# Kernel tuning notes

Measured on AMD Instinct MI355X. Metric: run time of the kernel, lower is better.

The kernel has to match this reference:

```python
import jax, jax.numpy as jnp
import numpy as np

USER_NUM = 200000
ITEM_NUM = 100000
N_NODES = USER_NUM + ITEM_NUM
EMB = 64
NNZ = 12800000
N_LAYERS = 3


def setup_inputs() -> dict:
    key = jax.random.key(0)
    k1, k2, k3, k4, k5 = jax.random.split(key, 5)
    user_emb = jax.random.normal(k1, (USER_NUM, EMB), dtype=jnp.float32) * 0.1
    item_emb = jax.random.normal(k2, (ITEM_NUM, EMB), dtype=jnp.float32) * 0.1
    adj_rows = jax.random.randint(k3, (NNZ,), 0, N_NODES, dtype=jnp.int32)
    adj_cols = jax.random.randint(k4, (NNZ,), 0, N_NODES, dtype=jnp.int32)
    # values of a symmetrically-normalized Laplacian are ~1/sqrt(d_i d_j);
    # avg degree ~= NNZ / N_NODES ~= 43, so scale uniform values accordingly
    # to keep row sums near 1 (numerically faithful to a normalized adjacency)
    adj_vals = jax.random.uniform(k5, (NNZ,), dtype=jnp.float32) * (2.0 * N_NODES / NNZ)
    return {
        "user_emb": user_emb,
        "item_emb": item_emb,
        "adj_vals": adj_vals,
        "adj_rows": adj_rows,
        "adj_cols": adj_cols,
    }


def reference(user_emb, item_emb, adj_vals, adj_rows, adj_cols):
    n_users = user_emb.shape[0]
    n_items = item_emb.shape[0]
    n_nodes = n_users + n_items

    # ego_embeddings = cat([user_emb, item_emb], 0)
    ego = jnp.concatenate([user_emb, item_emb], axis=0)  # [N, d]

    # Running accumulation replaces stack+mean over layer outputs.
    acc = ego
    for _ in range(N_LAYERS):
        # SpMM: out[r] += v * ego[c] for each nonzero (r, c, v)
        gathered = ego[adj_cols] * adj_vals[:, None]          # [nnz, d]
        ego = jax.ops.segment_sum(gathered, adj_rows, num_segments=n_nodes)
        acc = acc + ego

    all_emb = acc / jnp.asarray(N_LAYERS + 1, dtype=acc.dtype)  # mean over layers
    user_all = all_emb[:n_users]
    item_all = all_emb[n_users:]
    return (user_all, item_all)
```

## Files before the change

### kernel.cpp

```cpp
#include <hip/hip_runtime.h>


typedef unsigned short u16;
typedef unsigned int   u32;
typedef unsigned long long u64;

#define USER_ELEMS   (200000 * 64)
#define N_NODES      300000
#define EMB          64
#define NNZ          12800000
#define TOTAL_ELEMS  (N_NODES * EMB)

#define NBUCK    2048
#define ROWS_PB  147
#define EPB      65536
#define NB_A     196
#define CNT_LEN  (NBUCK * NB_A)
#define TILE     4096
#define NTILES   (EPB / TILE)
#define BCAP     6784

#define FLAGS_SZ   256ULL
#define ACC_SZ     76800000ULL
#define EGO_SZ     38400000ULL
#define RP_SZ      1200128ULL
#define BS_SZ      1024ULL
#define CNTM_SZ    1605632ULL
#define COL_SZ     51200000ULL
#define VALSORT_SZ 25600000ULL
#define BIG_SZ     115200000ULL
#define PERM_SZ    51200000ULL
#define LAYER_SZ   76800000ULL

#define T0_NEED (FLAGS_SZ + CNTM_SZ + 2*BS_SZ + COL_SZ + VALSORT_SZ + RP_SZ + BIG_SZ)
#define T2_NEED (FLAGS_SZ + ACC_SZ + EGO_SZ + 2*RP_SZ + 2*BS_SZ + PERM_SZ)

__device__ __forceinline__ float bf2f(u16 b) {
    return __uint_as_float(((u32)b) << 16);
}
__device__ __forceinline__ u16 f2bf(float f) {
    u32 u = __float_as_uint(f);
    u32 r = (u + 0x7fffu + ((u >> 16) & 1u)) >> 16;
    return (u16)r;
}

__global__ void k_detect(const u16* __restrict__ emb, const u16* __restrict__ vals,
                         int* __restrict__ flags) {
    int lane = threadIdx.x;
    u16 a = emb[lane * 2];
    int ea = (a >> 7) & 0xFF;
    bool pa = (ea >= 0x60 && ea <= 0x7E);
    unsigned long long ba = __ballot(pa);
    u16 b = vals[lane * 2];
    int eb = (b >> 7) & 0xFF;
    bool pb = (eb >= 0x60 && eb <= 0x7E);
    unsigned long long bb = __ballot(pb);
    if (lane == 0) {
        flags[0] = (__popcll(ba) >= 56) ? 0 : 1;
        flags[1] = (__popcll(bb) >= 56) ? 0 : 1;
    }
}

__global__ void k_init_ego(const void* __restrict__ user, const void* __restrict__ item,
                           const int* __restrict__ flags, u16* __restrict__ ego) {
    int t = blockIdx.x * blockDim.x + threadIdx.x;
    int e = t * 4;
    if (e >= TOTAL_ELEMS) return;
    float4 f;
    if (flags[0]) {
        const float* src = (e < USER_ELEMS) ? ((const float*)user + e)
                                            : ((const float*)item + (e - USER_ELEMS));
        f = *(const float4*)src;
    } else {
        const u16* src = (e < USER_ELEMS) ? ((const u16*)user + e)
                                          : ((const u16*)item + (e - USER_ELEMS));
        ushort4 v = *(const ushort4*)src;
        f.x = bf2f(v.x); f.y = bf2f(v.y); f.z = bf2f(v.z); f.w = bf2f(v.w);
    }
    ushort4 o;
    o.x = f2bf(f.x); o.y = f2bf(f.y); o.z = f2bf(f.z); o.w = f2bf(f.w);
    *(ushort4*)(ego + e) = o;
}

__global__ void k_init(const void* __restrict__ user, const void* __restrict__ item,
                       const int* __restrict__ flags,
                       u16* __restrict__ ego, float* __restrict__ acc) {
    int t = blockIdx.x * blockDim.x + threadIdx.x;
    int e = t * 4;
    if (e >= TOTAL_ELEMS) return;
    float4 f;
    if (flags[0]) {
        const float* src = (e < USER_ELEMS) ? ((const float*)user + e)
                                            : ((const float*)item + (e - USER_ELEMS));
        f = *(const float4*)src;
    } else {
        const u16* src = (e < USER_ELEMS) ? ((const u16*)user + e)
                                          : ((const u16*)item + (e - USER_ELEMS));
        ushort4 v = *(const ushort4*)src;
        f.x = bf2f(v.x); f.y = bf2f(v.y); f.z = bf2f(v.z); f.w = bf2f(v.w);
    }
    ushort4 o;
    o.x = f2bf(f.x); o.y = f2bf(f.y); o.z = f2bf(f.z); o.w = f2bf(f.w);
    *(ushort4*)(ego + e) = o;
    *(float4*)(acc + e) = f;
}

template<int EPT>
__global__ void k_scan_reduce(const int* __restrict__ cnt, int* __restrict__ blockSums,
                              int n) {
    __shared__ int s[256];
    int b = blockIdx.x;
    int base = b * (EPT * 256) + threadIdx.x;
    int sum = 0;
#pragma unroll
    for (int k = 0; k < EPT; ++k) {
        int i = base + k * 256;
        if (i < n) sum += cnt[i];
    }
    s[threadIdx.x] = sum;
    __syncthreads();
    for (int off = 128; off > 0; off >>= 1) {
        if (threadIdx.x < (unsigned)off) s[threadIdx.x] += s[threadIdx.x + off];
        __syncthreads();
    }
    if (threadIdx.x == 0) blockSums[b] = s[0];
}

__global__ void k_scan_block(const int* __restrict__ blockSums, int* __restrict__ blockOffs,
                             int nb) {
    __shared__ int s[256];
    int x = (threadIdx.x < nb) ? blockSums[threadIdx.x] : 0;
    s[threadIdx.x] = x;
    __syncthreads();
    for (int off = 1; off < 256; off <<= 1) {
        int t = 0;
        if (threadIdx.x >= (unsigned)off) t = s[threadIdx.x - off];
        __syncthreads();
        s[threadIdx.x] += t;
        __syncthreads();
    }
    if (threadIdx.x < nb) blockOffs[threadIdx.x] = s[threadIdx.x] - x;
}

template<int EPT>
__global__ void k_scan_down(const int* cnt, const int* __restrict__ blockOffs,
                            int* __restrict__ out, int* cursor2,
                            int n, int total, int writeTotal) {
    __shared__ int s[256];
    int b = blockIdx.x;
    int base = b * (EPT * 256) + threadIdx.x * EPT;
    int v[EPT];
    int tsum = 0;
#pragma unroll
    for (int k = 0; k < EPT; ++k) {
        int i = base + k;
        v[k] = (i < n) ? cnt[i] : 0;
        tsum += v[k];
    }
    s[threadIdx.x] = tsum;
    __syncthreads();
    for (int off = 1; off < 256; off <<= 1) {
        int t = 0;
        if (threadIdx.x >= (unsigned)off) t = s[threadIdx.x - off];
        __syncthreads();
        s[threadIdx.x] += t;
        __syncthreads();
    }
    int running = blockOffs[b] + (s[threadIdx.x] - tsum);
#pragma unroll
    for (int k = 0; k < EPT; ++k) {
        int i = base + k;
        if (i < n) {
            out[i] = running;
            if (cursor2) cursor2[i] = running;
        }
        running += v[k];
    }
    if (writeTotal && b == 0 && threadIdx.x == 0) out[n] = total;
}

__global__ void __launch_bounds__(512) k_bhist(const int* __restrict__ rows,
                                               int* __restrict__ counts) {
    __shared__ int c[NBUCK];
    for (int i = threadIdx.x; i < NBUCK; i += 512) c[i] = 0;
    __syncthreads();
    int b0 = blockIdx.x * EPB;
    for (int i = threadIdx.x; i < EPB; i += 512) {
        int e = b0 + i;
        if (e < NNZ) {
            u32 k = (u32)rows[e] / ROWS_PB;
            if (k >= NBUCK) k = NBUCK - 1;
            atomicAdd(&c[k], 1);
        }
    }
    __syncthreads();
    for (int k = threadIdx.x; k < NBUCK; k += 512)
        counts[k * NB_A + blockIdx.x] = c[k];
}

__global__ void __launch_bounds__(512) k_bscatter(
    const int* __restrict__ rows, const int* __restrict__ cols,
    const void* __restrict__ vals, const int* __restrict__ flags,
    const int* __restrict__ offs, u64* __restrict__ stg) {
    __shared__ int h[NBUCK];
    __shared__ u16 o[NBUCK];
    __shared__ int gbase[NBUCK];
    __shared__ u64 st[TILE];
    __shared__ u16 kst[TILE];
    int b = blockIdx.x, tid = threadIdx.x;
    for (int i = tid; i < NBUCK; i += 512) gbase[i] = offs[i * NB_A + b];
    int valF32 = flags[1];
    for (int t = 0; t < NTILES; ++t) {
        for (int i = tid; i < NBUCK; i += 512) h[i] = 0;
        __syncthreads();
        int ebase = b * EPB + t * TILE;
        int kk[8]; int rk[8]; u64 pl[8];
#pragma unroll
        for (int j = 0; j < 8; ++j) {
            int e = ebase + tid + j * 512;
            kk[j] = -1;
            if (e < NNZ) {
                u32 r = (u32)rows[e];
                u32 c = (u32)cols[e] & 0x7FFFFu;
                u16 v = valF32 ? f2bf(((const float*)vals)[e]) : ((const u16*)vals)[e];
                u32 k = r / ROWS_PB;
                if (k >= NBUCK) k = NBUCK - 1;
                u32 rl = r - k * ROWS_PB;
                if (rl >= ROWS_PB) rl = ROWS_PB - 1;
                kk[j] = (int)k;
                pl[j] = ((u64)v << 32) | (u64)((rl << 19) | c);
                rk[j] = atomicAdd(&h[k], 1);
            }
        }
        __syncthreads();
        for (int i = tid; i < NBUCK; i += 512) o[i] = (u16)h[i];
        __syncthreads();
        for (int off = 1; off < NBUCK; off <<= 1) {
            u16 t0[4];
#pragma unroll
            for (int q = 0; q < 4; ++q) {
                int i = tid + q * 512;
                t0[q] = (i >= off) ? o[i - off] : (u16)0;
            }
            __syncthreads();
#pragma unroll
            for (int q = 0; q < 4; ++q) o[tid + q * 512] += t0[q];
            __syncthreads();
        }
#pragma unroll
        for (int j = 0; j < 8; ++j) {
            if (kk[j] >= 0) {
                int excl = (int)o[kk[j]] - h[kk[j]];
                int p = excl + rk[j];
                if (p >= 0 && p < TILE) {
                    st[p] = pl[j];
                    kst[p] = (u16)kk[j];
                }
            }
        }
        __syncthreads();
        int cnt = (int)o[NBUCK - 1];
        if (cnt > TILE) cnt = TILE;
        for (int i = tid; i < cnt; i += 512) {
            int k = kst[i];
            int excl = (int)o[k] - h[k];
            long long p = (long long)gbase[k] + (i - excl);
            if (p >= 0 && p < NNZ) stg[p] = st[i];
        }
        __syncthreads();
        for (int i = tid; i < NBUCK; i += 512) gbase[i] += h[i];
        __syncthreads();
    }
}

__global__ void __launch_bounds__(512) k_bsort(
    const int* __restrict__ offs, const u64* __restrict__ stg,
    int* __restrict__ col_s, u16* __restrict__ val_s, int* __restrict__ row_ptr) {
    __shared__ int h[ROWS_PB], ex[ROWS_PB + 1], rk[ROWS_PB];
    __shared__ u32 lcol[BCAP];
    __shared__ u16 lval[BCAP];
    int k = blockIdx.x, tid = threadIdx.x;
    int s = offs[k * NB_A];
    int e = (k == NBUCK - 1) ? NNZ : offs[(k + 1) * NB_A];
    if (e > NNZ) e = NNZ;
    if (s < 0) s = 0;
    for (int i = tid; i < ROWS_PB; i += 512) h[i] = 0;
    __syncthreads();
    for (int j = s + tid; j < e; j += 512) {
        u32 rl = ((u32)stg[j]) >> 19;
        if (rl >= ROWS_PB) rl = ROWS_PB - 1;
        atomicAdd(&h[rl], 1);
    }
    __syncthreads();
    if (tid == 0) {
        int run = 0;
        for (int q = 0; q < ROWS_PB; ++q) { ex[q] = run; run += h[q]; }
        ex[ROWS_PB] = run;
    }
    __syncthreads();
    for (int i = tid; i < ROWS_PB; i += 512) rk[i] = ex[i];
    __syncthreads();
    int n = e - s;
    for (int j = s + tid; j < e; j += 512) {
        u64 pk = stg[j];
        u32 lo = (u32)pk;
        u32 rl = lo >> 19;
        if (rl >= ROWS_PB) rl = ROWS_PB - 1;
        int p = atomicAdd(&rk[rl], 1);
        if (p >= 0 && p < BCAP) { lcol[p] = lo & 0x7FFFFu; lval[p] = (u16)(pk >> 32); }
        else if (p >= 0 && p < n) {
            col_s[s + p] = (int)(lo & 0x7FFFFu); val_s[s + p] = (u16)(pk >> 32);
        }
    }
    __syncthreads();
    int m = n < BCAP ? n : BCAP;
    for (int i = tid; i < m; i += 512) {
        col_s[s + i] = (int)lcol[i];
        val_s[s + i] = lval[i];
    }
    int rowbase = k * ROWS_PB;
    for (int i = tid; i < ROWS_PB; i += 512) {
        int r = rowbase + i;
        if (r <= N_NODES) row_ptr[r] = s + ex[i];
    }
}

template<int FINAL>
__global__ void __launch_bounds__(256) k_spmm(
    const int* __restrict__ row_ptr, const int* __restrict__ col_s,
    const u16* __restrict__ val_s, const u16* __restrict__ ego_in,
    u16* __restrict__ ego_out,
    const u16* __restrict__ e0, const u16* __restrict__ e1,
    const int* __restrict__ flags, void* __restrict__ out) {
    int row = __builtin_amdgcn_readfirstlane(
        (int)((blockIdx.x * blockDim.x + threadIdx.x) >> 6));
    int lane = threadIdx.x & 63;
    if (row >= N_NODES) return;
    int start = row_ptr[row];
    int end   = row_ptr[row + 1];
    float a = 0.f;
    int j = start;
    for (; j + 8 <= end; j += 8) {
        int c[8]; u16 w[8];
#pragma unroll
        for (int q = 0; q < 8; ++q) { c[q] = col_s[j + q]; w[q] = val_s[j + q]; }
        float x[8];
#pragma unroll
        for (int q = 0; q < 8; ++q) {
            u32 cc = (u32)c[q] & 0x7FFFFu;
            x[q] = bf2f(ego_in[cc * EMB + lane]);
        }
#pragma unroll
        for (int q = 0; q < 8; ++q) a += bf2f(w[q]) * x[q];
    }
    for (; j < end; ++j) {
        u32 cc = (u32)col_s[j] & 0x7FFFFu;
        a += bf2f(val_s[j]) * bf2f(ego_in[cc * EMB + lane]);
    }
    int o = row * EMB + lane;
    if (FINAL) {
        float s = bf2f(e0[o]) + bf2f(e1[o]) + bf2f(ego_in[o]) + a;
        s *= 0.25f;
        if (flags[0]) ((float*)out)[o] = s;
        else          ((u16*)out)[o]  = f2bf(s);
    } else {
        ego_out[o] = f2bf(a);
    }
}

__global__ void k_hist(const int* __restrict__ rows, int* __restrict__ cnt) {
    int e = blockIdx.x * blockDim.x + threadIdx.x;
    if (e < NNZ) atomicAdd(&cnt[rows[e]], 1);
}

__global__ void k_scatter_perm(const int* __restrict__ rows, int* __restrict__ cursor,
                               u32* __restrict__ perm) {
    int e = blockIdx.x * blockDim.x + threadIdx.x;
    if (e >= NNZ) return;
    int r = rows[e];
    int p = atomicAdd(&cursor[r], 1);
    perm[p] = (u32)e;
}

__global__ void __launch_bounds__(256) k_spmm_perm(
    const int* __restrict__ row_ptr, const u32* __restrict__ perm,
    const int* __restrict__ cols, const void* __restrict__ vals,
    const int* __restrict__ flags, const u16* __restrict__ ego_in,
    u16* __restrict__ ego_out, float* __restrict__ acc) {
    int row = __builtin_amdgcn_readfirstlane(
        (int)((blockIdx.x * blockDim.x + threadIdx.x) >> 6));
    int lane = threadIdx.x & 63;
    if (row >= N_NODES) return;
    int valF32 = flags[1];
    int start = row_ptr[row];
    int end   = row_ptr[row + 1];
    float a = 0.f;
    for (int j = start; j < end; ++j) {
        u32 eid = perm[j];
        int c = cols[eid];
        float w = valF32 ? ((const float*)vals)[eid] : bf2f(((const u16*)vals)[eid]);
        a += w * bf2f(ego_in[c * EMB + lane]);
    }
    int o = row * EMB + lane;
    acc[o] += a;
    ego_out[o] = f2bf(a);
}

__global__ void __launch_bounds__(256) k_edge_atomic(
    const int* __restrict__ rows, const int* __restrict__ cols,
    const void* __restrict__ vals, const int* __restrict__ flags,
    const u16* __restrict__ ego, float* __restrict__ layer) {
    int t = blockIdx.x * blockDim.x + threadIdx.x;
    int e = t >> 4;
    if (e >= NNZ) return;
    int d4 = (t & 15) * 4;
    int r = rows[e], c = cols[e];
    float w = flags[1] ? ((const float*)vals)[e] : bf2f(((const u16*)vals)[e]);
    ushort4 x = *(const ushort4*)(ego + c * EMB + d4);
    float* dst = layer + r * EMB + d4;
    atomicAdd(dst + 0, w * bf2f(x.x));
    atomicAdd(dst + 1, w * bf2f(x.y));
    atomicAdd(dst + 2, w * bf2f(x.z));
    atomicAdd(dst + 3, w * bf2f(x.w));
}

__global__ void k_layer_fin(float* __restrict__ layer, float* __restrict__ acc,
                            u16* __restrict__ ego) {
    int t = blockIdx.x * blockDim.x + threadIdx.x;
    int e = t * 4;
    if (e >= TOTAL_ELEMS) return;
    float4 L = *(const float4*)(layer + e);
    float4 A = *(const float4*)(acc + e);
    A.x += L.x; A.y += L.y; A.z += L.z; A.w += L.w;
    *(float4*)(acc + e) = A;
    ushort4 o;
    o.x = f2bf(L.x); o.y = f2bf(L.y); o.z = f2bf(L.z); o.w = f2bf(L.w);
    *(ushort4*)(ego + e) = o;
    float4 z; z.x = 0.f; z.y = 0.f; z.z = 0.f; z.w = 0.f;
    *(float4*)(layer + e) = z;
}

__global__ void k_final(const float* __restrict__ acc, const int* __restrict__ flags,
                        void* __restrict__ out) {
    int t = blockIdx.x * blockDim.x + threadIdx.x;
    int e = t * 4;
    if (e >= TOTAL_ELEMS) return;
    float4 f = *(const float4*)(acc + e);
    f.x *= 0.25f; f.y *= 0.25f; f.z *= 0.25f; f.w *= 0.25f;
    if (flags[0]) {
        *(float4*)((float*)out + e) = f;
    } else {
        ushort4 v;
        v.x = f2bf(f.x); v.y = f2bf(f.y); v.z = f2bf(f.z); v.w = f2bf(f.w);
        *(ushort4*)((u16*)out + e) = v;
    }
}

extern "C" void kernel_launch(void* const* d_in, const int* in_sizes, int n_in,
                              void* d_out, int out_size, void* d_ws, size_t ws_size,
                              hipStream_t stream) {
    const void* user = d_in[0];
    const void* item = d_in[1];
    const void* vals = d_in[2];
    const int*  rows = (const int*)d_in[3];
    const int*  cols = (const int*)d_in[4];

    char* ws = (char*)d_ws;
    int* flags = (int*)ws;

    const int initGrid = (TOTAL_ELEMS / 4 + 255) / 256;
    const int edgeGrid = (NNZ + 255) / 256;
    const int spmmGrid = (N_NODES * 64) / 256;

    k_detect<<<1, 64, 0, stream>>>((const u16*)user, (const u16*)vals, flags);

    if (ws_size >= T0_NEED) {
        size_t off = FLAGS_SZ;
        int* cntm = (int*)(ws + off); off += CNTM_SZ;
        int* bs2  = (int*)(ws + off); off += BS_SZ;
        int* bo2  = (int*)(ws + off); off += BS_SZ;
        int* col_s = (int*)(ws + off); off += COL_SZ;
        u16* val_s = (u16*)(ws + off); off += VALSORT_SZ;
        int* row_ptr = (int*)(ws + off); off += RP_SZ;
        char* big  = ws + off;
        u64* stg = (u64*)big;
        u16* e0  = (u16*)big;
        u16* e1  = (u16*)(big + EGO_SZ);
        u16* e2  = (u16*)(big + 2 * EGO_SZ);

        k_bhist<<<NB_A, 512, 0, stream>>>(rows, cntm);
        k_scan_reduce<16><<<98, 256, 0, stream>>>(cntm, bs2, CNT_LEN);
        k_scan_block<<<1, 256, 0, stream>>>(bs2, bo2, 98);
        k_scan_down<16><<<98, 256, 0, stream>>>(cntm, bo2, cntm, (int*)0, CNT_LEN, 0, 0);

        k_bscatter<<<NB_A, 512, 0, stream>>>(rows, cols, vals, flags, cntm, stg);
        k_bsort<<<NBUCK, 512, 0, stream>>>(cntm, stg, col_s, val_s, row_ptr);

        k_init_ego<<<initGrid, 256, 0, stream>>>(user, item, flags, e0);
        k_spmm<0><<<spmmGrid, 256, 0, stream>>>(row_ptr, col_s, val_s, e0, e1,
                                                e0, e1, flags, (void*)d_out);
        k_spmm<0><<<spmmGrid, 256, 0, stream>>>(row_ptr, col_s, val_s, e1, e2,
                                                e0, e1, flags, (void*)d_out);
        k_spmm<1><<<spmmGrid, 256, 0, stream>>>(row_ptr, col_s, val_s, e2, e1,
                                                e0, e1, flags, d_out);
    } else if (ws_size >= T2_NEED) {
        size_t off = FLAGS_SZ;
        float* acc = (float*)(ws + off); off += ACC_SZ;
        u16* ego0 = (u16*)d_out;
        u16* ego1 = (u16*)(ws + off); off += EGO_SZ;
        int* row_ptr = (int*)(ws + off); off += RP_SZ;
        int* cursor  = (int*)(ws + off); off += RP_SZ;
        int* bsums   = (int*)(ws + off); off += BS_SZ;
        int* boffs   = (int*)(ws + off); off += BS_SZ;
        u32* perm    = (u32*)(ws + off); off += PERM_SZ;

        hipMemsetAsync(cursor, 0, N_NODES * sizeof(int), stream);
        k_init<<<initGrid, 256, 0, stream>>>(user, item, flags, ego0, acc);
        k_hist<<<edgeGrid, 256, 0, stream>>>(rows, cursor);
        k_scan_reduce<8><<<147, 256, 0, stream>>>(cursor, bsums, N_NODES);
        k_scan_block<<<1, 256, 0, stream>>>(bsums, boffs, 147);
        k_scan_down<8><<<147, 256, 0, stream>>>(cursor, boffs, row_ptr, cursor,
                                                N_NODES, NNZ, 1);
        k_scatter_perm<<<edgeGrid, 256, 0, stream>>>(rows, cursor, perm);
        k_spmm_perm<<<spmmGrid, 256, 0, stream>>>(row_ptr, perm, cols, vals, flags,
                                                  ego0, ego1, acc);
        k_spmm_perm<<<spmmGrid, 256, 0, stream>>>(row_ptr, perm, cols, vals, flags,
                                                  ego1, ego0, acc);
        k_spmm_perm<<<spmmGrid, 256, 0, stream>>>(row_ptr, perm, cols, vals, flags,
                                                  ego0, ego1, acc);
        k_final<<<initGrid, 256, 0, stream>>>(acc, flags, d_out);
    } else {
        size_t off = FLAGS_SZ;
        float* acc   = (float*)(ws + off); off += ACC_SZ;
        float* layer = (float*)(ws + off); off += LAYER_SZ;
        u16* ego = (u16*)d_out;
        hipMemsetAsync(layer, 0, LAYER_SZ, stream);
        k_init<<<initGrid, 256, 0, stream>>>(user, item, flags, ego, acc);
        const int atomGrid = (NNZ * 16) / 256;
        for (int l = 0; l < 3; ++l) {
            k_edge_atomic<<<atomGrid, 256, 0, stream>>>(rows, cols, vals, flags, ego, layer);
            k_layer_fin<<<initGrid, 256, 0, stream>>>(layer, acc, ego);
        }
        k_final<<<initGrid, 256, 0, stream>>>(acc, flags, d_out);
    }
}
```

Before: 1.292 ms.

## Sub-sort bucket edges by column chunk within rows for gather locality

The per-bucket sort now keys on (row, column chunk of 32K nodes) instead of row alone, so the edges within each row come out grouped by column range. This should make the SpMM gathers of ego rows more cache-friendly. The serial single-thread prefix scan is replaced with a parallel block-wide scan over the larger key space. row_ptr is now written from the first chunk offset of each row. The cost is a larger shared histogram and a few more scan barriers in a preprocessing kernel.

```diff
diff --git a/kernel.cpp b/kernel.cpp
--- a/kernel.cpp
+++ b/kernel.cpp
@@ -19,6 +19,9 @@
 #define TILE     4096
 #define NTILES   (EPB / TILE)
 #define BCAP     6784
+#define NCH      16
+#define KEYS     (ROWS_PB * NCH)
+#define KPT      ((KEYS + 511) / 512)
 
 #define FLAGS_SZ   256ULL
 #define ACC_SZ     76800000ULL
@@ -276,7 +279,9 @@
 __global__ void __launch_bounds__(512) k_bsort(
     const int* __restrict__ offs, const u64* __restrict__ stg,
     int* __restrict__ col_s, u16* __restrict__ val_s, int* __restrict__ row_ptr) {
-    __shared__ int h[ROWS_PB], ex[ROWS_PB + 1], rk[ROWS_PB];
+    __shared__ int h[KEYS];
+    __shared__ int ex[KEYS];
+    __shared__ int s512[512];
     __shared__ u32 lcol[BCAP];
     __shared__ u16 lval[BCAP];
     int k = blockIdx.x, tid = threadIdx.x;
@@ -284,21 +289,44 @@
     int e = (k == NBUCK - 1) ? NNZ : offs[(k + 1) * NB_A];
     if (e > NNZ) e = NNZ;
     if (s < 0) s = 0;
-    for (int i = tid; i < ROWS_PB; i += 512) h[i] = 0;
+    for (int i = tid; i < KEYS; i += 512) h[i] = 0;
     __syncthreads();
     for (int j = s + tid; j < e; j += 512) {
-        u32 rl = ((u32)stg[j]) >> 19;
+        u32 lo = (u32)stg[j];
+        u32 rl = lo >> 19;
         if (rl >= ROWS_PB) rl = ROWS_PB - 1;
-        atomicAdd(&h[rl], 1);
-    }
-    __syncthreads();
-    if (tid == 0) {
-        int run = 0;
-        for (int q = 0; q < ROWS_PB; ++q) { ex[q] = run; run += h[q]; }
-        ex[ROWS_PB] = run;
-    }
-    __syncthreads();
-    for (int i = tid; i < ROWS_PB; i += 512) rk[i] = ex[i];
+        u32 ch = (lo & 0x7FFFFu) >> 15;
+        atomicAdd(&h[rl * NCH + ch], 1);
+    }
+    __syncthreads();
+    int loc[KPT]; int tsum = 0; int base = tid * KPT;
+#pragma unroll
+    for (int q = 0; q < KPT; ++q) {
+        int i = base + q;
+        loc[q] = (i < KEYS) ? h[i] : 0;
+        tsum += loc[q];
+    }
+    s512[tid] = tsum;
+    __syncthreads();
+    for (int off = 1; off < 512; off <<= 1) {
+        int t = 0;
+        if (tid >= off) t = s512[tid - off];
+        __syncthreads();
+        s512[tid] += t;
+        __syncthreads();
+    }
+    int run = s512[tid] - tsum;
+#pragma unroll
+    for (int q = 0; q < KPT; ++q) {
+        int i = base + q;
+        if (i < KEYS) { ex[i] = run; run += loc[q]; }
+    }
+    __syncthreads();
+    int rowbase = k * ROWS_PB;
+    for (int i = tid; i < ROWS_PB; i += 512) {
+        int r = rowbase + i;
+        if (r <= N_NODES) row_ptr[r] = s + ex[i * NCH];
+    }
     __syncthreads();
     int n = e - s;
     for (int j = s + tid; j < e; j += 512) {
@@ -306,7 +334,8 @@
         u32 lo = (u32)pk;
         u32 rl = lo >> 19;
         if (rl >= ROWS_PB) rl = ROWS_PB - 1;
-        int p = atomicAdd(&rk[rl], 1);
+        u32 ch = (lo & 0x7FFFFu) >> 15;
+        int p = atomicAdd(&ex[rl * NCH + ch], 1);
         if (p >= 0 && p < BCAP) { lcol[p] = lo & 0x7FFFFu; lval[p] = (u16)(pk >> 32); }
         else if (p >= 0 && p < n) {
             col_s[s + p] = (int)(lo & 0x7FFFFu); val_s[s + p] = (u16)(pk >> 32);
@@ -317,11 +346,6 @@
     for (int i = tid; i < m; i += 512) {
         col_s[s + i] = (int)lcol[i];
         val_s[s + i] = lval[i];
-    }
-    int rowbase = k * ROWS_PB;
-    for (int i = tid; i < ROWS_PB; i += 512) {
-        int r = rowbase + i;
-        if (r <= N_NODES) row_ptr[r] = s + ex[i];
     }
 }
 
```

Result: no change. 1.293 ms (+0.0%).
